# Kernel tuning notes

Measured on AMD Instinct MI355X. Metric: run time of the kernel, lower is better.

The kernel has to match this reference:

```python
import jax, jax.numpy as jnp
import numpy as np

D_MODEL = 1024
N_HEADS = 16
D_K = D_MODEL // N_HEADS


def setup_inputs() -> dict:
    key = jax.random.key(0)
    k1, k2, k3 = jax.random.split(key, 3)
    x = jax.random.normal(k1, (4, 2048, D_MODEL), dtype=jnp.float32)
    # torch nn.Linear(d_model, 3*d_model, bias=False): y = x @ W.T, W: [3D, D].
    # We store transposed weights [D, 3D] so y = x @ W_attn (same math).
    scale = 1.0 / np.sqrt(D_MODEL)
    W_attn = jax.random.uniform(k2, (D_MODEL, 3 * D_MODEL), dtype=jnp.float32, minval=-scale, maxval=scale)
    W_proj = jax.random.uniform(k3, (D_MODEL, D_MODEL), dtype=jnp.float32, minval=-scale, maxval=scale)
    return {"x": x, "W_attn": W_attn, "W_proj": W_proj}


def reference(x, W_attn, W_proj):
    B, S, D = x.shape
    qkv = x @ W_attn                       # [B, S, 3D]
    q, k, v = jnp.split(qkv, 3, axis=-1)   # each [B, S, D]
    # [B, S, D] -> [B, H, S, d_k]
    def heads(t):
        return t.reshape(B, S, N_HEADS, D_K).transpose(0, 2, 1, 3)
    q, k, v = heads(q), heads(k), heads(v)
    scores = jnp.einsum('bhqd,bhkd->bhqk', q, k) / jnp.sqrt(jnp.float32(D_K))
    weights = jax.nn.softmax(scores, axis=-1)
    attn = jnp.einsum('bhqk,bhkd->bhqd', weights, v)  # [B, H, S, d_k]
    attn = attn.transpose(0, 2, 1, 3).reshape(B, S, D)
    return attn @ W_proj
```

## Files before the change

kernel.cpp:

```cpp
#include <hip/hip_runtime.h>
#include <hip/hip_bf16.h>

#define D_MODEL 1024
#define N_HEADS 16
#define SEQ     2048
#define BATCH   4
#define CSC     (0.125f * 1.44269504f)

typedef __attribute__((ext_vector_type(8))) short short8;
typedef __attribute__((ext_vector_type(4))) float f32x4;

__device__ __forceinline__ ushort f2bf(float v) {
    __hip_bfloat16 b = __float2bfloat16(v);
    return __builtin_bit_cast(ushort, b);
}
__device__ __forceinline__ float bf2f(ushort u) {
    return __bfloat162float(__builtin_bit_cast(__hip_bfloat16, u));
}
__device__ __forceinline__ void splitf(float v, ushort& h, ushort& l) {
    h = f2bf(v);
    l = f2bf(v - bf2f(h));
}
__device__ __forceinline__ f32x4 mfma16(short8 a, short8 b, f32x4 c) {
    return __builtin_amdgcn_mfma_f32_16x16x32_bf16(a, b, c, 0, 0, 0);
}
__device__ __forceinline__ void gload_lds16(const ushort* g, ushort* l) {
    __builtin_amdgcn_global_load_lds(
        (const __attribute__((address_space(1))) unsigned int*)g,
        (__attribute__((address_space(3))) unsigned int*)l, 16, 0, 0);
}

__global__ __launch_bounds__(256) void split_x_k(const float4* __restrict__ x,
                                                 ushort4* __restrict__ xh, int n4) {
    for (int i = blockIdx.x * blockDim.x + threadIdx.x; i < n4;
         i += gridDim.x * blockDim.x) {
        float4 v = x[i];
        ushort4 hv;
        hv.x = f2bf(v.x);
        hv.y = f2bf(v.y);
        hv.z = f2bf(v.z);
        hv.w = f2bf(v.w);
        xh[i] = hv;
    }
}

__global__ __launch_bounds__(256) void split_wt_k(const float* __restrict__ W,
                                                  ushort* __restrict__ WhT,
                                                  ushort* __restrict__ WlT,
                                                  int K, int N, int writeLo,
                                                  float scale, int scale_nmax) {
    __shared__ float tile[32][33];
    const int kb = blockIdx.y * 32, nb = blockIdx.x * 32;
    const int tx = threadIdx.x, ty = threadIdx.y;
#pragma unroll
    for (int i = 0; i < 4; ++i)
        tile[ty + 8 * i][tx] = W[(size_t)(kb + ty + 8 * i) * N + nb + tx];
    __syncthreads();
#pragma unroll
    for (int i = 0; i < 4; ++i) {
        int n = nb + ty + 8 * i;
        float v = tile[tx][ty + 8 * i];
        if (n < scale_nmax) v *= scale;
        ushort h, l;
        splitf(v, h, l);
        size_t o = (size_t)n * K + kb + tx;
        WhT[o] = h;
        if (writeLo) WlT[o] = l;
    }
}

__global__ __launch_bounds__(256) void transpose_v_k(const ushort* __restrict__ qkv_h,
                                                     ushort* __restrict__ vT_h) {
    __shared__ ushort th[64][68];
    const int st = blockIdx.x, h = blockIdx.y, b = blockIdx.z;
    const int t = threadIdx.x;
    const int s0 = st * 64;
    {
        int s = t >> 2, dc = (t & 3) * 16;
        const size_t src = ((size_t)(b * SEQ + s0 + s)) * 3072 + 2048 + h * 64 + dc;
        *(uint4*)&th[s][dc]     = *(const uint4*)&qkv_h[src];
        *(uint4*)&th[s][dc + 8] = *(const uint4*)&qkv_h[src + 8];
    }
    __syncthreads();
    {
        int d = t >> 2, sc = (t & 3) * 16;
        ushort bufh[16];
#pragma unroll
        for (int j = 0; j < 16; ++j) bufh[j] = th[sc + j][d];
        const size_t dst = ((size_t)((b * 16 + h) * 64 + d)) * SEQ + s0 + sc;
        *(uint4*)&vT_h[dst]     = *(uint4*)&bufh[0];
        *(uint4*)&vT_h[dst + 8] = *(uint4*)&bufh[8];
    }
}

template <int OUT_SPLIT, int TERMS>
__global__ __launch_bounds__(256) void gemm_k(
    const ushort* __restrict__ Ah, int lda, int aoff,
    const ushort* __restrict__ BhT, const ushort* __restrict__ BlT,
    ushort* __restrict__ Ch, float* __restrict__ Cf,
    int ldc, int coff, int K) {
    constexpr int NT = TERMS + 1;
    __shared__ __align__(16) ushort lds[2][NT][4096];
    const int t = threadIdx.x;
    const int lane = t & 63, wid = t >> 6;
    const int wm = (wid >> 1) * 64, wn = (wid & 1) * 64;
    const int row0 = blockIdx.y * 128, col0 = blockIdx.x * 128;

    f32x4 acc[4][4];
#pragma unroll
    for (int i = 0; i < 4; ++i)
#pragma unroll
        for (int j = 0; j < 4; ++j) acc[i][j] = f32x4{0.f, 0.f, 0.f, 0.f};

    const int r_loc = lane >> 2;
    const int c_src = (lane & 3) ^ ((lane >> 3) & 3);
    const int swz = ((lane & 15) >> 1) & 3;
    const int ch = (((lane >> 4) ^ swz) * 8);
    const int rA = wm + (lane & 15);
    const int rB = wn + (lane & 15);

    auto stage = [&](int buf, int kk) {
#pragma unroll
        for (int ic = 0; ic < 2 * NT; ++ic) {
            const int c = wid * 2 * NT + ic;
            const int tile = c >> 3, chi = c & 7;
            const ushort* s;
            int sr, sl, so;
            if (tile == 0)      { s = Ah;  sr = row0; sl = lda; so = aoff; }
            else if (tile == 1) { s = BhT; sr = col0; sl = K;   so = 0; }
            else                { s = BlT; sr = col0; sl = K;   so = 0; }
            const ushort* gp =
                s + (size_t)(sr + chi * 16 + r_loc) * sl + so + kk + c_src * 8;
            gload_lds16(gp, &lds[buf][tile][chi * 512 + 0]);
        }
    };

    stage(0, 0);
    for (int k0 = 0; k0 < K; k0 += 32) {
        const int cur = (k0 >> 5) & 1;
        if (k0 + 32 < K) {
            stage(cur ^ 1, k0 + 32);
            if constexpr (TERMS == 1)
                asm volatile("s_waitcnt vmcnt(4)" ::: "memory");
            else
                asm volatile("s_waitcnt vmcnt(6)" ::: "memory");
        } else {
            asm volatile("s_waitcnt vmcnt(0)" ::: "memory");
        }
        __builtin_amdgcn_s_barrier();
        __builtin_amdgcn_sched_barrier(0);

        short8 ah[4], bh[4];
#pragma unroll
        for (int f = 0; f < 4; ++f) {
            ah[f] = *(const short8*)&lds[cur][0][(rA + f * 16) * 32 + ch];
            bh[f] = *(const short8*)&lds[cur][1][(rB + f * 16) * 32 + ch];
        }
        __builtin_amdgcn_s_setprio(1);
#pragma unroll
        for (int i = 0; i < 4; ++i)
#pragma unroll
            for (int j = 0; j < 4; ++j) acc[i][j] = mfma16(ah[i], bh[j], acc[i][j]);
        __builtin_amdgcn_s_setprio(0);
        if (TERMS >= 2) {
            short8 bl[4];
#pragma unroll
            for (int f = 0; f < 4; ++f)
                bl[f] = *(const short8*)&lds[cur][2][(rB + f * 16) * 32 + ch];
            __builtin_amdgcn_s_setprio(1);
#pragma unroll
            for (int i = 0; i < 4; ++i)
#pragma unroll
                for (int j = 0; j < 4; ++j) acc[i][j] = mfma16(ah[i], bl[j], acc[i][j]);
            __builtin_amdgcn_s_setprio(0);
        }
        asm volatile("s_waitcnt lgkmcnt(0)" ::: "memory");
        __builtin_amdgcn_s_barrier();
        __builtin_amdgcn_sched_barrier(0);
    }
#pragma unroll
    for (int i = 0; i < 4; ++i)
#pragma unroll
        for (int j = 0; j < 4; ++j)
#pragma unroll
            for (int r = 0; r < 4; ++r) {
                int row = row0 + wm + i * 16 + (lane >> 4) * 4 + r;
                int col = col0 + wn + j * 16 + (lane & 15);
                float v = acc[i][j][r];
                if (OUT_SPLIT) {
                    Ch[(size_t)row * ldc + coff + col] = f2bf(v);
                } else {
                    Cf[(size_t)row * ldc + coff + col] = v;
                }
            }
}

__global__ __launch_bounds__(512) void flash_mfma(
    const ushort* __restrict__ qkv_h, const ushort* __restrict__ vT_h,
    ushort* __restrict__ attn_h) {
    const int id = blockIdx.x;
    const int bh = id & 63, qt = id >> 6;
    const int h = bh & 15, b = bh >> 4;
    const int t = threadIdx.x, lane = t & 63, wid = t >> 6;
    const int q = lane & 15, g = lane >> 4;
    const int qs7 = q & 7;

    __shared__ __align__(16) ushort Kb[2][4096];
    __shared__ __align__(16) ushort Vb[2][4096];
    __shared__ __align__(16) ushort Pb[8][1024];

    const size_t tokbase = (size_t)b * SEQ;
    const int q0 = qt * 128;
    const int kv_r = lane >> 3;
    const int kv_csrc = (lane & 7) ^ ((lane >> 3) & 7);
    const size_t vbase = ((size_t)(b * 16 + h) * 64) * SEQ;

    ushort* KQ = &Kb[0][0];
#pragma unroll
    for (int is = 0; is < 2; ++is) {
        int ci = wid * 2 + is;
        const ushort* gq =
            qkv_h + (tokbase + q0 + ci * 8 + kv_r) * 3072 + h * 64 + kv_csrc * 8;
        gload_lds16(gq, KQ + ci * 512);
    }
    __syncthreads();
    const int ck0 = (g ^ qs7) * 8;
    const int ck1 = ((g + 4) ^ qs7) * 8;
    short8 qh[2];
    {
        const int row = wid * 16 + q;
        qh[0] = *(const short8*)&KQ[row * 64 + ck0];
        qh[1] = *(const short8*)&KQ[row * 64 + ck1];
    }
    __syncthreads();

    const int qck0 = q * 64 + ck0;
    const int qck1 = q * 64 + ck1;
    ushort* Pw = &Pb[wid][0];
    const int pw0 = q * 64 + (((g >> 1) + 0) ^ qs7) * 8 + (g & 1) * 4;
    const int pw1 = q * 64 + (((g >> 1) + 2) ^ qs7) * 8 + (g & 1) * 4;
    const int pw2 = q * 64 + (((g >> 1) + 4) ^ qs7) * 8 + (g & 1) * 4;
    const int pw3 = q * 64 + (((g >> 1) + 6) ^ qs7) * 8 + (g & 1) * 4;

    auto stage = [&](int buf, int kv0) {
        if (wid < 4) {
            const ushort* gsrc =
                qkv_h + (tokbase + kv0 + wid * 16) * 3072 + 1024 + h * 64;
            ushort* dst = &Kb[buf][wid * 1024];
#pragma unroll
            for (int is = 0; is < 2; ++is)
                gload_lds16(gsrc + (size_t)(is * 8 + kv_r) * 3072 + kv_csrc * 8,
                            dst + is * 512);
        } else {
            const ushort* gsrc = vT_h + vbase + (size_t)((wid - 4) * 16) * SEQ + kv0;
            ushort* dst = &Vb[buf][(wid - 4) * 1024];
#pragma unroll
            for (int is = 0; is < 2; ++is)
                gload_lds16(gsrc + (size_t)(is * 8 + kv_r) * SEQ + kv_csrc * 8,
                            dst + is * 512);
        }
    };

    stage(0, 0);

    float l_ = 0.f;
    f32x4 o[4];
#pragma unroll
    for (int i = 0; i < 4; ++i) o[i] = f32x4{0.f, 0.f, 0.f, 0.f};

    auto body = [&](int cur) {
        const ushort* Kc = &Kb[cur][0];
        const ushort* Vc = &Vb[cur][0];

        f32x4 s[4];
#pragma unroll
        for (int j = 0; j < 4; ++j) s[j] = f32x4{0.f, 0.f, 0.f, 0.f};
        __builtin_amdgcn_s_setprio(1);
#pragma unroll
        for (int j = 0; j < 4; ++j) {
            short8 kh0 = *(const short8*)&Kc[j * 1024 + qck0];
            s[j] = mfma16(kh0, qh[0], s[j]);
            short8 kh1 = *(const short8*)&Kc[j * 1024 + qck1];
            s[j] = mfma16(kh1, qh[1], s[j]);
        }
        __builtin_amdgcn_s_setprio(0);

        float rs = 0.f;
#pragma unroll
        for (int j = 0; j < 4; ++j) {
            ushort4 hv;
            float p0 = __builtin_exp2f(s[j][0]);
            float p1 = __builtin_exp2f(s[j][1]);
            float p2 = __builtin_exp2f(s[j][2]);
            float p3 = __builtin_exp2f(s[j][3]);
            rs += (p0 + p1) + (p2 + p3);
            hv.x = f2bf(p0);
            hv.y = f2bf(p1);
            hv.z = f2bf(p2);
            hv.w = f2bf(p3);
            const int off = (j == 0) ? pw0 : (j == 1) ? pw1 : (j == 2) ? pw2 : pw3;
            *(ushort4*)&Pw[off] = hv;
        }
        l_ += rs;
        asm volatile("s_waitcnt lgkmcnt(0)" ::: "memory");
        __builtin_amdgcn_sched_barrier(0);

        __builtin_amdgcn_s_setprio(1);
#pragma unroll
        for (int ks = 0; ks < 2; ++ks) {
            short8 pa = *(const short8*)&Pw[ks ? qck1 : qck0];
#pragma unroll
            for (int jp = 0; jp < 4; ++jp) {
                short8 vh = *(const short8*)&Vc[jp * 1024 + (ks ? qck1 : qck0)];
                o[jp] = mfma16(pa, vh, o[jp]);
            }
        }
        __builtin_amdgcn_s_setprio(0);

        asm volatile("s_waitcnt lgkmcnt(0)" ::: "memory");
        __builtin_amdgcn_s_barrier();
        __builtin_amdgcn_sched_barrier(0);
    };

    for (int kt2 = 0; kt2 < SEQ / 128; ++kt2) {
        stage(1, (kt2 * 2 + 1) * 64);
        asm volatile("s_waitcnt vmcnt(2)" ::: "memory");
        __builtin_amdgcn_s_barrier();
        __builtin_amdgcn_sched_barrier(0);
        body(0);
        if (kt2 < SEQ / 128 - 1) {
            stage(0, (kt2 * 2 + 2) * 64);
            asm volatile("s_waitcnt vmcnt(2)" ::: "memory");
        } else {
            asm volatile("s_waitcnt vmcnt(0)" ::: "memory");
        }
        __builtin_amdgcn_s_barrier();
        __builtin_amdgcn_sched_barrier(0);
        body(1);
    }

    l_ += __shfl_xor(l_, 16);
    l_ += __shfl_xor(l_, 32);
    float inv = 1.f / l_;
#pragma unroll
    for (int r = 0; r < 4; ++r) {
        float invr = __shfl(inv, (g << 2) + r);
        int tok = q0 + wid * 16 + g * 4 + r;
        size_t rowb = (tokbase + tok) * 3072;
#pragma unroll
        for (int jp = 0; jp < 4; ++jp) {
            int col = h * 64 + jp * 16 + q;
            attn_h[rowb + col] = f2bf(o[jp][r] * invr);
        }
    }
}


extern "C" void kernel_launch(void* const* d_in, const int* in_sizes, int n_in,
                              void* d_out, int out_size, void* d_ws, size_t ws_size,
                              hipStream_t stream) {
    const float* x      = (const float*)d_in[0];
    const float* W_attn = (const float*)d_in[1];
    const float* W_proj = (const float*)d_in[2];

    const int M = BATCH * SEQ;

    ushort* qkv_h = (ushort*)d_ws;
    ushort* W_h   = qkv_h + (size_t)M * 3072;

    ushort* xh   = (ushort*)d_out;
    ushort* vT_h = (ushort*)d_out;

    split_x_k<<<2048, 256, 0, stream>>>((const float4*)x, (ushort4*)xh, M * 1024 / 4);
    split_wt_k<<<dim3(96, 32), dim3(32, 8), 0, stream>>>(W_attn, W_h, nullptr,
                                                         1024, 3072, 0, CSC, 1024);
    gemm_k<1, 1><<<dim3(24, 64), 256, 0, stream>>>(xh, 1024, 0, W_h, nullptr,
                                                   qkv_h, nullptr, 3072, 0, 1024);
    transpose_v_k<<<dim3(32, 16, 4), 256, 0, stream>>>(qkv_h, vT_h);
    split_wt_k<<<dim3(32, 32), dim3(32, 8), 0, stream>>>(W_proj, W_h, nullptr,
                                                         1024, 1024, 0, 1.0f, 0);
    flash_mfma<<<dim3(1024), 512, 0, stream>>>(qkv_h, vT_h, qkv_h + 2048);
    gemm_k<0, 1><<<dim3(8, 64), 256, 0, stream>>>(qkv_h, 3072, 2048, W_h, nullptr,
                                                  nullptr, (float*)d_out, 1024, 0,
                                                  1024);
}
```

Baseline: 226.1 us.

## Fuse prep kernels into one launch and single-buffer V in flash attention

```diff
diff --git a/kernel.cpp b/kernel.cpp
--- a/kernel.cpp
+++ b/kernel.cpp
@@ -14,13 +14,6 @@
     __hip_bfloat16 b = __float2bfloat16(v);
     return __builtin_bit_cast(ushort, b);
 }
-__device__ __forceinline__ float bf2f(ushort u) {
-    return __bfloat162float(__builtin_bit_cast(__hip_bfloat16, u));
-}
-__device__ __forceinline__ void splitf(float v, ushort& h, ushort& l) {
-    h = f2bf(v);
-    l = f2bf(v - bf2f(h));
-}
 __device__ __forceinline__ f32x4 mfma16(short8 a, short8 b, f32x4 c) {
     return __builtin_amdgcn_mfma_f32_16x16x32_bf16(a, b, c, 0, 0, 0);
 }
@@ -30,42 +23,47 @@
         (__attribute__((address_space(3))) unsigned int*)l, 16, 0, 0);
 }
 
-__global__ __launch_bounds__(256) void split_x_k(const float4* __restrict__ x,
-                                                 ushort4* __restrict__ xh, int n4) {
-    for (int i = blockIdx.x * blockDim.x + threadIdx.x; i < n4;
-         i += gridDim.x * blockDim.x) {
-        float4 v = x[i];
-        ushort4 hv;
-        hv.x = f2bf(v.x);
-        hv.y = f2bf(v.y);
-        hv.z = f2bf(v.z);
-        hv.w = f2bf(v.w);
-        xh[i] = hv;
-    }
-}
-
-__global__ __launch_bounds__(256) void split_wt_k(const float* __restrict__ W,
-                                                  ushort* __restrict__ WhT,
-                                                  ushort* __restrict__ WlT,
-                                                  int K, int N, int writeLo,
-                                                  float scale, int scale_nmax) {
-    __shared__ float tile[32][33];
-    const int kb = blockIdx.y * 32, nb = blockIdx.x * 32;
-    const int tx = threadIdx.x, ty = threadIdx.y;
-#pragma unroll
-    for (int i = 0; i < 4; ++i)
-        tile[ty + 8 * i][tx] = W[(size_t)(kb + ty + 8 * i) * N + nb + tx];
-    __syncthreads();
-#pragma unroll
-    for (int i = 0; i < 4; ++i) {
-        int n = nb + ty + 8 * i;
-        float v = tile[tx][ty + 8 * i];
-        if (n < scale_nmax) v *= scale;
-        ushort h, l;
-        splitf(v, h, l);
-        size_t o = (size_t)n * K + kb + tx;
-        WhT[o] = h;
-        if (writeLo) WlT[o] = l;
+__global__ __launch_bounds__(256) void prep_k(const float* __restrict__ x,
+                                              const float* __restrict__ Wa,
+                                              const float* __restrict__ Wp,
+                                              ushort* __restrict__ xh,
+                                              ushort* __restrict__ WaT,
+                                              ushort* __restrict__ WpT) {
+    const int id = blockIdx.x;
+    const int t = threadIdx.x;
+    if (id < 2048) {
+        const float4* x4 = (const float4*)x;
+        ushort4* xh4 = (ushort4*)xh;
+        const int n4 = BATCH * SEQ * D_MODEL / 4;
+        for (int i = id * 256 + t; i < n4; i += 2048 * 256) {
+            float4 v = x4[i];
+            ushort4 hv;
+            hv.x = f2bf(v.x);
+            hv.y = f2bf(v.y);
+            hv.z = f2bf(v.z);
+            hv.w = f2bf(v.w);
+            xh4[i] = hv;
+        }
+    } else {
+        __shared__ float tile[32][33];
+        const float* W;
+        ushort* WT;
+        int N, tid, scaleQ;
+        if (id < 2048 + 3072) { tid = id - 2048; W = Wa; WT = WaT; N = 3072; scaleQ = 1; }
+        else                  { tid = id - 5120; W = Wp; WT = WpT; N = 1024; scaleQ = 0; }
+        const int nb = (tid % (N / 32)) * 32, kb = (tid / (N / 32)) * 32;
+        const int tx = t & 31, ty = t >> 5;
+#pragma unroll
+        for (int i = 0; i < 4; ++i)
+            tile[ty + 8 * i][tx] = W[(size_t)(kb + ty + 8 * i) * N + nb + tx];
+        __syncthreads();
+#pragma unroll
+        for (int i = 0; i < 4; ++i) {
+            int n = nb + ty + 8 * i;
+            float v = tile[tx][ty + 8 * i];
+            if (scaleQ && n < 1024) v *= CSC;
+            WT[(size_t)n * 1024 + kb + tx] = f2bf(v);
+        }
     }
 }
 
@@ -93,14 +91,13 @@
     }
 }
 
-template <int OUT_SPLIT, int TERMS>
+template <int OUT_SPLIT>
 __global__ __launch_bounds__(256) void gemm_k(
     const ushort* __restrict__ Ah, int lda, int aoff,
-    const ushort* __restrict__ BhT, const ushort* __restrict__ BlT,
+    const ushort* __restrict__ BhT,
     ushort* __restrict__ Ch, float* __restrict__ Cf,
     int ldc, int coff, int K) {
-    constexpr int NT = TERMS + 1;
-    __shared__ __align__(16) ushort lds[2][NT][4096];
+    __shared__ __align__(16) ushort lds[2][2][4096];
     const int t = threadIdx.x;
     const int lane = t & 63, wid = t >> 6;
     const int wm = (wid >> 1) * 64, wn = (wid & 1) * 64;
@@ -121,14 +118,13 @@
 
     auto stage = [&](int buf, int kk) {
 #pragma unroll
-        for (int ic = 0; ic < 2 * NT; ++ic) {
-            const int c = wid * 2 * NT + ic;
+        for (int ic = 0; ic < 4; ++ic) {
+            const int c = wid * 4 + ic;
             const int tile = c >> 3, chi = c & 7;
-            const ushort* s;
-            int sr, sl, so;
-            if (tile == 0)      { s = Ah;  sr = row0; sl = lda; so = aoff; }
-            else if (tile == 1) { s = BhT; sr = col0; sl = K;   so = 0; }
-            else                { s = BlT; sr = col0; sl = K;   so = 0; }
+            const ushort* s = tile ? BhT : Ah;
+            const int sr = tile ? col0 : row0;
+            const int sl = tile ? K : lda;
+            const int so = tile ? 0 : aoff;
             const ushort* gp =
                 s + (size_t)(sr + chi * 16 + r_loc) * sl + so + kk + c_src * 8;
             gload_lds16(gp, &lds[buf][tile][chi * 512 + 0]);
@@ -140,10 +136,7 @@
         const int cur = (k0 >> 5) & 1;
         if (k0 + 32 < K) {
             stage(cur ^ 1, k0 + 32);
-            if constexpr (TERMS == 1)
-                asm volatile("s_waitcnt vmcnt(4)" ::: "memory");
-            else
-                asm volatile("s_waitcnt vmcnt(6)" ::: "memory");
+            asm volatile("s_waitcnt vmcnt(4)" ::: "memory");
         } else {
             asm volatile("s_waitcnt vmcnt(0)" ::: "memory");
         }
@@ -162,18 +155,6 @@
 #pragma unroll
             for (int j = 0; j < 4; ++j) acc[i][j] = mfma16(ah[i], bh[j], acc[i][j]);
         __builtin_amdgcn_s_setprio(0);
-        if (TERMS >= 2) {
-            short8 bl[4];
-#pragma unroll
-            for (int f = 0; f < 4; ++f)
-                bl[f] = *(const short8*)&lds[cur][2][(rB + f * 16) * 32 + ch];
-            __builtin_amdgcn_s_setprio(1);
-#pragma unroll
-            for (int i = 0; i < 4; ++i)
-#pragma unroll
-                for (int j = 0; j < 4; ++j) acc[i][j] = mfma16(ah[i], bl[j], acc[i][j]);
-            __builtin_amdgcn_s_setprio(0);
-        }
         asm volatile("s_waitcnt lgkmcnt(0)" ::: "memory");
         __builtin_amdgcn_s_barrier();
         __builtin_amdgcn_sched_barrier(0);
@@ -206,7 +187,7 @@
     const int qs7 = q & 7;
 
     __shared__ __align__(16) ushort Kb[2][4096];
-    __shared__ __align__(16) ushort Vb[2][4096];
+    __shared__ __align__(16) ushort Vb[4096];
     __shared__ __align__(16) ushort Pb[8][1024];
 
     const size_t tokbase = (size_t)b * SEQ;
@@ -242,26 +223,25 @@
     const int pw2 = q * 64 + (((g >> 1) + 4) ^ qs7) * 8 + (g & 1) * 4;
     const int pw3 = q * 64 + (((g >> 1) + 6) ^ qs7) * 8 + (g & 1) * 4;
 
-    auto stage = [&](int buf, int kv0) {
-        if (wid < 4) {
-            const ushort* gsrc =
-                qkv_h + (tokbase + kv0 + wid * 16) * 3072 + 1024 + h * 64;
-            ushort* dst = &Kb[buf][wid * 1024];
-#pragma unroll
-            for (int is = 0; is < 2; ++is)
-                gload_lds16(gsrc + (size_t)(is * 8 + kv_r) * 3072 + kv_csrc * 8,
-                            dst + is * 512);
-        } else {
-            const ushort* gsrc = vT_h + vbase + (size_t)((wid - 4) * 16) * SEQ + kv0;
-            ushort* dst = &Vb[buf][(wid - 4) * 1024];
-#pragma unroll
-            for (int is = 0; is < 2; ++is)
-                gload_lds16(gsrc + (size_t)(is * 8 + kv_r) * SEQ + kv_csrc * 8,
-                            dst + is * 512);
-        }
+    auto stageK = [&](int buf, int kv0) {
+        const ushort* gsrc =
+            qkv_h + (tokbase + kv0 + wid * 16) * 3072 + 1024 + h * 64;
+        ushort* dst = &Kb[buf][wid * 1024];
+#pragma unroll
+        for (int is = 0; is < 2; ++is)
+            gload_lds16(gsrc + (size_t)(is * 8 + kv_r) * 3072 + kv_csrc * 8,
+                        dst + is * 512);
     };
-
-    stage(0, 0);
+    auto stageV = [&](int kv0) {
+        const ushort* gsrc = vT_h + vbase + (size_t)((wid - 4) * 16) * SEQ + kv0;
+        ushort* dst = &Vb[(wid - 4) * 1024];
+#pragma unroll
+        for (int is = 0; is < 2; ++is)
+            gload_lds16(gsrc + (size_t)(is * 8 + kv_r) * SEQ + kv_csrc * 8,
+                        dst + is * 512);
+    };
+
+    if (wid < 4) stageK(0, 0); else stageV(0);
 
     float l_ = 0.f;
     f32x4 o[4];
@@ -270,7 +250,6 @@
 
     auto body = [&](int cur) {
         const ushort* Kc = &Kb[cur][0];
-        const ushort* Vc = &Vb[cur][0];
 
         f32x4 s[4];
 #pragma unroll
@@ -311,7 +290,7 @@
             short8 pa = *(const short8*)&Pw[ks ? qck1 : qck0];
 #pragma unroll
             for (int jp = 0; jp < 4; ++jp) {
-                short8 vh = *(const short8*)&Vc[jp * 1024 + (ks ? qck1 : qck0)];
+                short8 vh = *(const short8*)&Vb[jp * 1024 + (ks ? qck1 : qck0)];
                 o[jp] = mfma16(pa, vh, o[jp]);
             }
         }
@@ -323,20 +302,30 @@
     };
 
     for (int kt2 = 0; kt2 < SEQ / 128; ++kt2) {
-        stage(1, (kt2 * 2 + 1) * 64);
-        asm volatile("s_waitcnt vmcnt(2)" ::: "memory");
-        __builtin_amdgcn_s_barrier();
-        __builtin_amdgcn_sched_barrier(0);
-        body(0);
-        if (kt2 < SEQ / 128 - 1) {
-            stage(0, (kt2 * 2 + 2) * 64);
+        if (wid < 4) {
+            stageK(1, (kt2 * 2 + 1) * 64);
             asm volatile("s_waitcnt vmcnt(2)" ::: "memory");
         } else {
             asm volatile("s_waitcnt vmcnt(0)" ::: "memory");
         }
         __builtin_amdgcn_s_barrier();
         __builtin_amdgcn_sched_barrier(0);
+        body(0);
+        if (wid >= 4) stageV((kt2 * 2 + 1) * 64);
+        if (wid < 4) {
+            if (kt2 < SEQ / 128 - 1) {
+                stageK(0, (kt2 * 2 + 2) * 64);
+                asm volatile("s_waitcnt vmcnt(2)" ::: "memory");
+            } else {
+                asm volatile("s_waitcnt vmcnt(0)" ::: "memory");
+            }
+        } else {
+            asm volatile("s_waitcnt vmcnt(0)" ::: "memory");
+        }
+        __builtin_amdgcn_s_barrier();
+        __builtin_amdgcn_sched_barrier(0);
         body(1);
+        if (wid >= 4 && kt2 < SEQ / 128 - 1) stageV((kt2 * 2 + 2) * 64);
     }
 
     l_ += __shfl_xor(l_, 16);
@@ -366,21 +355,18 @@
     const int M = BATCH * SEQ;
 
     ushort* qkv_h = (ushort*)d_ws;
-    ushort* W_h   = qkv_h + (size_t)M * 3072;
+    ushort* WaT   = qkv_h + (size_t)M * 3072;
+    ushort* WpT   = WaT + (size_t)3072 * 1024;
 
     ushort* xh   = (ushort*)d_out;
     ushort* vT_h = (ushort*)d_out;
 
-    split_x_k<<<2048, 256, 0, stream>>>((const float4*)x, (ushort4*)xh, M * 1024 / 4);
-    split_wt_k<<<dim3(96, 32), dim3(32, 8), 0, stream>>>(W_attn, W_h, nullptr,
-                                                         1024, 3072, 0, CSC, 1024);
-    gemm_k<1, 1><<<dim3(24, 64), 256, 0, stream>>>(xh, 1024, 0, W_h, nullptr,
-                                                   qkv_h, nullptr, 3072, 0, 1024);
+    prep_k<<<dim3(6144), 256, 0, stream>>>(x, W_attn, W_proj, xh, WaT, WpT);
+    gemm_k<1><<<dim3(24, 64), 256, 0, stream>>>(xh, 1024, 0, WaT,
+                                                qkv_h, nullptr, 3072, 0, 1024);
     transpose_v_k<<<dim3(32, 16, 4), 256, 0, stream>>>(qkv_h, vT_h);
-    split_wt_k<<<dim3(32, 32), dim3(32, 8), 0, stream>>>(W_proj, W_h, nullptr,
-                                                         1024, 1024, 0, 1.0f, 0);
     flash_mfma<<<dim3(1024), 512, 0, stream>>>(qkv_h, vT_h, qkv_h + 2048);
-    gemm_k<0, 1><<<dim3(8, 64), 256, 0, stream>>>(qkv_h, 3072, 2048, W_h, nullptr,
-                                                  nullptr, (float*)d_out, 1024, 0,
-                                                  1024);
-}
+    gemm_k<0><<<dim3(8, 64), 256, 0, stream>>>(qkv_h, 3072, 2048, WpT,
+                                               nullptr, (float*)d_out, 1024, 0,
+                                               1024);
+}
```

Measured after the change: 225.7 us. No clear change (-0.2%).
